# Optimization experiments

Measured on AMD Instinct MI355X. Metric: run time of the kernel, lower is better.

Reference implementation:

```python
import jax, jax.numpy as jnp
import numpy as np
from jax import lax

H = 1024        # lstm_hidden_size
V = 512         # action_vocab_size
WV = 300        # word_vec_size
S = 64          # step_num
N = 512         # entity_num


def setup_inputs() -> dict:
    key = jax.random.key(0)
    ks = jax.random.split(key, 16)
    s = 0.02
    return {
        "video_vectors": jax.random.normal(ks[0], (1, S, H), jnp.float32),
        "entity_vectors": jax.random.normal(ks[1], (N, H), jnp.float32),
        # action_selector: Linear(H,H) -> ReLU -> Dropout(eval: identity) -> Linear(H,V) -> Sigmoid
        "A1w": jax.random.normal(ks[2], (H, H), jnp.float32) * s,
        "A1b": jnp.zeros((H,), jnp.float32),
        "A2w": jax.random.normal(ks[3], (V, H), jnp.float32) * s,
        "A2b": jnp.zeros((V,), jnp.float32),
        "action_emb": jax.random.normal(ks[4], (V, WV), jnp.float32) * s,
        "W1w": jax.random.normal(ks[5], (H, H), jnp.float32) * s,
        "W1b": jnp.zeros((H,), jnp.float32),
        "W2w": jax.random.normal(ks[6], (H, H + V), jnp.float32) * s,
        "W2b": jnp.zeros((H,), jnp.float32),
        "W3w": jax.random.normal(ks[7], (3, H), jnp.float32) * s,
        "W3b": jnp.zeros((3,), jnp.float32),
        "W4w": jax.random.normal(ks[8], (1, WV), jnp.float32) * s,
        "W4b": jnp.zeros((1,), jnp.float32),
    }


def _forward(video_vectors, entity_vectors, A1w, A1b, A2w, A2b, action_emb,
             W1w, W1b, W2w, W2b, W3w, W3b, W4w, W4b):
    vv = video_vectors[0]                       # [S, H]
    n = entity_vectors.shape[0]

    def step(carry, v_ac):
        ev, prev_ent_attn = carry               # ev: [N, H], prev: [N]
        # action selector (dropout is identity in eval)
        h = jax.nn.relu(v_ac @ A1w.T + A1b)
        ac_prob = jax.nn.sigmoid(h @ A2w.T + A2b)        # [V]
        bar_ft = (ac_prob / ac_prob.sum()) @ action_emb  # [WV]
        hat_ht = jax.nn.relu(v_ac @ W1w.T + W1b)         # [H]
        w2v = jnp.concatenate([hat_ht, ac_prob]) @ W2w.T + W2b  # [H]
        ent_prob = jax.nn.sigmoid(ev @ w2v)              # [N]
        choice = jax.nn.softmax(hat_ht @ W3w.T + W3b)    # [3]
        attn = choice[0] * ent_prob + choice[1] * prev_ent_attn  # (choice[2]*0)
        bar_et = (attn / attn.sum()) @ ev                # [H]
        scal = bar_ft @ W4w[0] + W4b[0]                  # scalar (W4(bar_ft))
        kt = jax.nn.relu(scal * bar_et)                  # [H]
        ev_new = attn[:, None] * kt[None, :] + (1.0 - attn)[:, None] * ev  # [N, H]
        return (ev_new, ent_prob), (ent_prob, ac_prob, bar_et, ev_new, bar_ft)

    init = (entity_vectors, jnp.zeros((n,), entity_vectors.dtype))
    _, (ent_probs, ac_probs, step_ent, step_all, step_act) = lax.scan(step, init, vv)
    return ent_probs, ac_probs, step_ent, step_all, step_act


def reference(video_vectors, entity_vectors, A1w, A1b, A2w, A2b, action_emb,
              W1w, W1b, W2w, W2b, W3w, W3b, W4w, W4b):
    return _forward(video_vectors, entity_vectors, A1w, A1b, A2w, A2b, action_emb,
                    W1w, W1b, W2w, W2b, W3w, W3b, W4w, W4b)
```

## Files before the change

### kernel.cpp

```cpp
#include <hip/hip_runtime.h>

#define H  1024
#define V  512
#define WV 300
#define S  64
#define N  512

#define WS_HALL   0
#define WS_HAT    (S*H)
#define WS_W2V    (2*S*H)
#define WS_CHOICE (3*S*H)
#define WS_SCAL   (3*S*H + 2*S)
#define WS_ACSUM  (3*S*H + 3*S)
#define WS_ACCUM  (3*S*H + 4*S)
#define WS_ASUM   (WS_ACCUM + 3*H)
#define WS_CTR    (WS_ASUM + 4)
#define WS_FLOATS (WS_CTR + 1)

#define OUT_EP   0
#define OUT_AC   (S*N)
#define OUT_SE   (S*N + S*V)
#define OUT_ALL  (OUT_SE + S*H)
#define OUT_ACT  (OUT_ALL + (size_t)S*N*H)

__device__ __forceinline__ float wave_reduce(float v) {
#pragma unroll
  for (int m = 32; m > 0; m >>= 1) v += __shfl_xor(v, m, 64);
  return v;
}
__device__ __forceinline__ float dot4(float4 a, float4 b) {
  return a.x*b.x + a.y*b.y + a.z*b.z + a.w*b.w;
}

__global__ void k_vvmats(const float* __restrict__ vv,
                         const float* __restrict__ A1w, const float* __restrict__ A1b,
                         const float* __restrict__ W1w, const float* __restrict__ W1b,
                         float* __restrict__ ws) {
  int wid  = (blockIdx.x * blockDim.x + threadIdx.x) >> 6;
  int lane = threadIdx.x & 63;
  if (wid >= 2 * S * H) return;
  int mat = wid / (S * H);
  int rem = wid - mat * S * H;
  int t = rem >> 10, j = rem & (H - 1);
  const float* w = (mat ? W1w : A1w) + (size_t)j * H;
  const float* x = vv + (size_t)t * H;
  float sum = 0.f;
#pragma unroll
  for (int c = 0; c < 4; ++c) {
    float4 a = *(const float4*)(w + c*256 + lane*4);
    float4 b = *(const float4*)(x + c*256 + lane*4);
    sum += dot4(a, b);
  }
  sum = wave_reduce(sum);
  if (lane == 0) {
    float bias = (mat ? W1b : A1b)[j];
    ws[(mat ? WS_HAT : WS_HALL) + rem] = fmaxf(sum + bias, 0.f);
  }
}

__global__ void k_ac(const float* __restrict__ ws, const float* __restrict__ A2w,
                     const float* __restrict__ A2b, float* __restrict__ out_ac) {
  int wid  = (blockIdx.x * blockDim.x + threadIdx.x) >> 6;
  int lane = threadIdx.x & 63;
  if (wid >= S * V) return;
  int t = wid >> 9, v = wid & (V - 1);
  const float* h = ws + WS_HALL + (size_t)t * H;
  const float* w = A2w + (size_t)v * H;
  float sum = 0.f;
#pragma unroll
  for (int c = 0; c < 4; ++c) {
    float4 a = *(const float4*)(w + c*256 + lane*4);
    float4 b = *(const float4*)(h + c*256 + lane*4);
    sum += dot4(a, b);
  }
  sum = wave_reduce(sum);
  if (lane == 0) out_ac[wid] = 1.f / (1.f + __expf(-(sum + A2b[v])));
}

__global__ void k_choice(const float* __restrict__ ws_ro, const float* __restrict__ out_ac,
                         const float* __restrict__ W3w, const float* __restrict__ W3b,
                         float* __restrict__ ws) {
  int t = blockIdx.x, tid = threadIdx.x;
  const float* hat = ws_ro + WS_HAT + (size_t)t * H;
  float4 h4 = *(const float4*)(hat + tid * 4);
  float p[4];
#pragma unroll
  for (int r = 0; r < 3; ++r) {
    float4 w4 = *(const float4*)(W3w + (size_t)r * H + tid * 4);
    p[r] = dot4(h4, w4);
  }
  const float* ac = out_ac + (size_t)t * V;
  p[3] = ac[tid * 2] + ac[tid * 2 + 1];
  __shared__ float red[4][256];
#pragma unroll
  for (int q = 0; q < 4; ++q) red[q][tid] = p[q];
  __syncthreads();
  for (int sft = 128; sft > 0; sft >>= 1) {
    if (tid < sft) {
#pragma unroll
      for (int q = 0; q < 4; ++q) red[q][tid] += red[q][tid + sft];
    }
    __syncthreads();
  }
  if (tid == 0) {
    float l0 = red[0][0] + W3b[0], l1 = red[1][0] + W3b[1], l2 = red[2][0] + W3b[2];
    float m  = fmaxf(l0, fmaxf(l1, l2));
    float e0 = __expf(l0 - m), e1 = __expf(l1 - m), e2 = __expf(l2 - m);
    float inv = 1.f / (e0 + e1 + e2);
    ws[WS_CHOICE + t * 2]     = e0 * inv;
    ws[WS_CHOICE + t * 2 + 1] = e1 * inv;
    ws[WS_ACSUM + t]          = red[3][0];
  }
}

__global__ void k_w2v(const float* __restrict__ ws_ro, const float* __restrict__ out_ac,
                      const float* __restrict__ W2w, const float* __restrict__ W2b,
                      float* __restrict__ ws) {
  int wid  = (blockIdx.x * blockDim.x + threadIdx.x) >> 6;
  int lane = threadIdx.x & 63;
  if (wid >= S * H) return;
  int t = wid >> 10, j = wid & (H - 1);
  const float* w   = W2w + (size_t)j * (H + V);
  const float* hat = ws_ro + WS_HAT + (size_t)t * H;
  const float* ac  = out_ac + (size_t)t * V;
  float sum = 0.f;
#pragma unroll
  for (int c = 0; c < 4; ++c) {
    float4 a = *(const float4*)(w + c*256 + lane*4);
    float4 b = *(const float4*)(hat + c*256 + lane*4);
    sum += dot4(a, b);
  }
#pragma unroll
  for (int c = 0; c < 2; ++c) {
    float4 a = *(const float4*)(w + H + c*256 + lane*4);
    float4 b = *(const float4*)(ac + c*256 + lane*4);
    sum += dot4(a, b);
  }
  sum = wave_reduce(sum);
  if (lane == 0) ws[WS_W2V + wid] = sum + W2b[j];
}

__global__ void k_barft(const float* __restrict__ out_ac, const float* __restrict__ emb,
                        const float* __restrict__ ws_ro, float* __restrict__ out_act) {
  int wid  = (blockIdx.x * blockDim.x + threadIdx.x) >> 6;
  int lane = threadIdx.x & 63;
  if (wid >= S * WV) return;
  int t = wid / WV, w = wid - t * WV;
  const float* ac = out_ac + (size_t)t * V;
  float sum = 0.f;
  for (int v = lane; v < V; v += 64) sum += ac[v] * emb[(size_t)v * WV + w];
  sum = wave_reduce(sum);
  if (lane == 0) out_act[wid] = sum / ws_ro[WS_ACSUM + t];
}

__global__ void k_scal(const float* __restrict__ out_act, const float* __restrict__ W4w,
                       const float* __restrict__ W4b, float* __restrict__ ws) {
  int wid  = (blockIdx.x * blockDim.x + threadIdx.x) >> 6;
  int lane = threadIdx.x & 63;
  if (wid >= S) return;
  const float* bf = out_act + (size_t)wid * WV;
  float sum = 0.f;
  for (int w = lane; w < WV; w += 64) sum += bf[w] * W4w[w];
  sum = wave_reduce(sum);
  if (lane == 0) ws[WS_SCAL + wid] = sum + W4b[0];
}

__global__ __launch_bounds__(256) void k_seq(
    const float* __restrict__ ev0, const float* __restrict__ ws,
    float* __restrict__ accum, float* __restrict__ asum, unsigned* __restrict__ ctr,
    float* __restrict__ out_ep, float* __restrict__ out_se, float* __restrict__ out_all) {
  const int g = blockIdx.x, tid = threadIdx.x;
  const int lane = tid & 63, wv = tid >> 6;
  const int col = tid * 4;
  __shared__ float attnS[8], prevS[8], red[8][4];
  if (tid < 8) prevS[tid] = 0.f;
  float4 ev[8];
#pragma unroll
  for (int r = 0; r < 8; ++r)
    ev[r] = *(const float4*)(ev0 + (size_t)(g * 8 + r) * H + col);
  __syncthreads();
  unsigned target = 0;
  for (int t = 0; t < S; ++t) {
    const float4 w4 = *(const float4*)(ws + WS_W2V + (size_t)t * H + col);
    float dp[8];
#pragma unroll
    for (int r = 0; r < 8; ++r) dp[r] = dot4(ev[r], w4);
#pragma unroll
    for (int r = 0; r < 8; ++r) {
#pragma unroll
      for (int m = 32; m > 0; m >>= 1) dp[r] += __shfl_xor(dp[r], m, 64);
    }
    if (lane == 0) {
#pragma unroll
      for (int r = 0; r < 8; ++r) red[r][wv] = dp[r];
    }
    __syncthreads();
    if (tid < 8) {
      float d  = red[tid][0] + red[tid][1] + red[tid][2] + red[tid][3];
      float ep = 1.f / (1.f + __expf(-d));
      out_ep[(size_t)t * N + g * 8 + tid] = ep;
      float a = ws[WS_CHOICE + 2 * t] * ep + ws[WS_CHOICE + 2 * t + 1] * prevS[tid];
      prevS[tid] = ep;
      attnS[tid] = a;
    }
    __syncthreads();
    float at[8];
#pragma unroll
    for (int r = 0; r < 8; ++r) at[r] = attnS[r];
    float4 pv = make_float4(0.f, 0.f, 0.f, 0.f);
#pragma unroll
    for (int r = 0; r < 8; ++r) {
      pv.x += at[r] * ev[r].x; pv.y += at[r] * ev[r].y;
      pv.z += at[r] * ev[r].z; pv.w += at[r] * ev[r].w;
    }
    float* acc = accum + (t % 3) * H;
    atomicAdd(acc + col + 0, pv.x);
    atomicAdd(acc + col + 1, pv.y);
    atomicAdd(acc + col + 2, pv.z);
    atomicAdd(acc + col + 3, pv.w);
    if (tid == 0) {
      float pa = 0.f;
#pragma unroll
      for (int r = 0; r < 8; ++r) pa += at[r];
      atomicAdd(asum + (t % 3), pa);
    }
    __threadfence();
    __syncthreads();
    target += (unsigned)gridDim.x;
    if (tid == 0) {
      __hip_atomic_fetch_add(ctr, 1u, __ATOMIC_RELEASE, __HIP_MEMORY_SCOPE_AGENT);
      while (__hip_atomic_load(ctr, __ATOMIC_ACQUIRE, __HIP_MEMORY_SCOPE_AGENT) < target)
        __builtin_amdgcn_s_sleep(2);
    }
    __syncthreads();
    float asv = __hip_atomic_load(asum + (t % 3), __ATOMIC_RELAXED, __HIP_MEMORY_SCOPE_AGENT);
    float4 pvs;
    pvs.x = __hip_atomic_load(acc + col + 0, __ATOMIC_RELAXED, __HIP_MEMORY_SCOPE_AGENT);
    pvs.y = __hip_atomic_load(acc + col + 1, __ATOMIC_RELAXED, __HIP_MEMORY_SCOPE_AGENT);
    pvs.z = __hip_atomic_load(acc + col + 2, __ATOMIC_RELAXED, __HIP_MEMORY_SCOPE_AGENT);
    pvs.w = __hip_atomic_load(acc + col + 3, __ATOMIC_RELAXED, __HIP_MEMORY_SCOPE_AGENT);
    float inv = 1.f / asv;
    float4 bar = make_float4(pvs.x * inv, pvs.y * inv, pvs.z * inv, pvs.w * inv);
    float sc = ws[WS_SCAL + t];
    float4 kt = make_float4(fmaxf(sc * bar.x, 0.f), fmaxf(sc * bar.y, 0.f),
                            fmaxf(sc * bar.z, 0.f), fmaxf(sc * bar.w, 0.f));
    if (g == 0) *(float4*)(out_se + (size_t)t * H + col) = bar;
    if (tid < 16)
      __hip_atomic_store(accum + ((t + 2) % 3) * H + g * 16 + tid, 0.f,
                         __ATOMIC_RELAXED, __HIP_MEMORY_SCOPE_AGENT);
    if (g == 0 && tid == 16)
      __hip_atomic_store(asum + ((t + 2) % 3), 0.f, __ATOMIC_RELAXED, __HIP_MEMORY_SCOPE_AGENT);
    float* outp = out_all + (size_t)t * N * H;
#pragma unroll
    for (int r = 0; r < 8; ++r) {
      float a = at[r];
      ev[r].x = a * kt.x + (1.f - a) * ev[r].x;
      ev[r].y = a * kt.y + (1.f - a) * ev[r].y;
      ev[r].z = a * kt.z + (1.f - a) * ev[r].z;
      ev[r].w = a * kt.w + (1.f - a) * ev[r].w;
      *(float4*)(outp + (size_t)(g * 8 + r) * H + col) = ev[r];
    }
  }
}

extern "C" void kernel_launch(void* const* d_in, const int* in_sizes, int n_in,
                              void* d_out, int out_size, void* d_ws, size_t ws_size,
                              hipStream_t stream) {
  const float* vv  = (const float*)d_in[0];
  const float* ev0 = (const float*)d_in[1];
  const float* A1w = (const float*)d_in[2];
  const float* A1b = (const float*)d_in[3];
  const float* A2w = (const float*)d_in[4];
  const float* A2b = (const float*)d_in[5];
  const float* emb = (const float*)d_in[6];
  const float* W1w = (const float*)d_in[7];
  const float* W1b = (const float*)d_in[8];
  const float* W2w = (const float*)d_in[9];
  const float* W2b = (const float*)d_in[10];
  const float* W3w = (const float*)d_in[11];
  const float* W3b = (const float*)d_in[12];
  const float* W4w = (const float*)d_in[13];
  const float* W4b = (const float*)d_in[14];

  float* ws  = (float*)d_ws;
  float* out = (float*)d_out;
  float* out_ep  = out + OUT_EP;
  float* out_ac  = out + OUT_AC;
  float* out_se  = out + OUT_SE;
  float* out_all = out + OUT_ALL;
  float* out_act = out + OUT_ACT;

  hipMemsetAsync(ws + WS_ACCUM, 0, (size_t)(3 * H + 4 + 1) * sizeof(float), stream);

  k_vvmats<<<(2 * S * H) / 4, 256, 0, stream>>>(vv, A1w, A1b, W1w, W1b, ws);
  k_ac    <<<(S * V) / 4,     256, 0, stream>>>(ws, A2w, A2b, out_ac);
  k_choice<<<S,               256, 0, stream>>>(ws, out_ac, W3w, W3b, ws);
  k_w2v   <<<(S * H) / 4,     256, 0, stream>>>(ws, out_ac, W2w, W2b, ws);
  k_barft <<<(S * WV + 3) / 4, 256, 0, stream>>>(out_ac, emb, ws, out_act);
  k_scal  <<<(S + 3) / 4,     256, 0, stream>>>(out_act, W4w, W4b, ws);
  k_seq   <<<64,              256, 0, stream>>>(ev0, ws,
                                                ws + WS_ACCUM, ws + WS_ASUM,
                                                (unsigned*)(ws + WS_CTR),
                                                out_ep, out_se, out_all);
}
```

Before: 1.177 ms.

## Tile precompute GEMMs in LDS and move ev output writes to a separate kernel

```diff
diff --git a/kernel.cpp b/kernel.cpp
--- a/kernel.cpp
+++ b/kernel.cpp
@@ -7,15 +7,16 @@
 #define N  512
 
 #define WS_HALL   0
-#define WS_HAT    (S*H)
-#define WS_W2V    (2*S*H)
-#define WS_CHOICE (3*S*H)
-#define WS_SCAL   (3*S*H + 2*S)
-#define WS_ACSUM  (3*S*H + 3*S)
-#define WS_ACCUM  (3*S*H + 4*S)
+#define WS_CAT    (S*H)
+#define WS_W2V    (WS_CAT + S*1536)
+#define WS_CHOICE (WS_W2V + S*H)
+#define WS_SCAL   (WS_CHOICE + 2*S)
+#define WS_ACSUM  (WS_SCAL + S)
+#define WS_KT     (WS_ACSUM + S)
+#define WS_ATT    (WS_KT + S*H)
+#define WS_ACCUM  (WS_ATT + S*N)
 #define WS_ASUM   (WS_ACCUM + 3*H)
 #define WS_CTR    (WS_ASUM + 4)
-#define WS_FLOATS (WS_CTR + 1)
 
 #define OUT_EP   0
 #define OUT_AC   (S*N)
@@ -32,56 +33,72 @@
   return a.x*b.x + a.y*b.y + a.z*b.z + a.w*b.w;
 }
 
-__global__ void k_vvmats(const float* __restrict__ vv,
-                         const float* __restrict__ A1w, const float* __restrict__ A1b,
-                         const float* __restrict__ W1w, const float* __restrict__ W1b,
-                         float* __restrict__ ws) {
-  int wid  = (blockIdx.x * blockDim.x + threadIdx.x) >> 6;
-  int lane = threadIdx.x & 63;
-  if (wid >= 2 * S * H) return;
-  int mat = wid / (S * H);
-  int rem = wid - mat * S * H;
-  int t = rem >> 10, j = rem & (H - 1);
-  const float* w = (mat ? W1w : A1w) + (size_t)j * H;
-  const float* x = vv + (size_t)t * H;
-  float sum = 0.f;
-#pragma unroll
-  for (int c = 0; c < 4; ++c) {
-    float4 a = *(const float4*)(w + c*256 + lane*4);
-    float4 b = *(const float4*)(x + c*256 + lane*4);
-    sum += dot4(a, b);
-  }
-  sum = wave_reduce(sum);
-  if (lane == 0) {
-    float bias = (mat ? W1b : A1b)[j];
-    ws[(mat ? WS_HAT : WS_HALL) + rem] = fmaxf(sum + bias, 0.f);
-  }
-}
-
-__global__ void k_ac(const float* __restrict__ ws, const float* __restrict__ A2w,
-                     const float* __restrict__ A2b, float* __restrict__ out_ac) {
-  int wid  = (blockIdx.x * blockDim.x + threadIdx.x) >> 6;
-  int lane = threadIdx.x & 63;
-  if (wid >= S * V) return;
-  int t = wid >> 9, v = wid & (V - 1);
-  const float* h = ws + WS_HALL + (size_t)t * H;
-  const float* w = A2w + (size_t)v * H;
-  float sum = 0.f;
-#pragma unroll
-  for (int c = 0; c < 4; ++c) {
-    float4 a = *(const float4*)(w + c*256 + lane*4);
-    float4 b = *(const float4*)(h + c*256 + lane*4);
-    sum += dot4(a, b);
-  }
-  sum = wave_reduce(sum);
-  if (lane == 0) out_ac[wid] = 1.f / (1.f + __expf(-(sum + A2b[v])));
-}
-
-__global__ void k_choice(const float* __restrict__ ws_ro, const float* __restrict__ out_ac,
+#define KC 64
+__global__ __launch_bounds__(256) void gemmNT(
+    const float* __restrict__ X, int ldx,
+    const float* __restrict__ W, const float* __restrict__ bias,
+    int K, int act,
+    float* __restrict__ out1, int ld1,
+    float* __restrict__ out2, int ld2) {
+  __shared__ float Xs[64][KC + 4];
+  __shared__ float Ws[64][KC + 4];
+  const int tid = threadIdx.x;
+  const int tm = tid >> 5, tn = tid & 31;
+  const int jbase = blockIdx.x * 64;
+  float acc[8][2];
+#pragma unroll
+  for (int i = 0; i < 8; ++i) acc[i][0] = acc[i][1] = 0.f;
+  const int lr = tid >> 2;
+  const int lc = (tid & 3) * 16;
+  for (int k0 = 0; k0 < K; k0 += KC) {
+    const float4* xp = (const float4*)(X + (size_t)lr * ldx + k0 + lc);
+    const float4* wp = (const float4*)(W + (size_t)(jbase + lr) * K + k0 + lc);
+    float4 xv0 = xp[0], xv1 = xp[1], xv2 = xp[2], xv3 = xp[3];
+    float4 wv0 = wp[0], wv1 = wp[1], wv2 = wp[2], wv3 = wp[3];
+    __syncthreads();
+    *(float4*)&Xs[lr][lc +  0] = xv0; *(float4*)&Xs[lr][lc +  4] = xv1;
+    *(float4*)&Xs[lr][lc +  8] = xv2; *(float4*)&Xs[lr][lc + 12] = xv3;
+    *(float4*)&Ws[lr][lc +  0] = wv0; *(float4*)&Ws[lr][lc +  4] = wv1;
+    *(float4*)&Ws[lr][lc +  8] = wv2; *(float4*)&Ws[lr][lc + 12] = wv3;
+    __syncthreads();
+#pragma unroll
+    for (int kk = 0; kk < KC; kk += 4) {
+      float4 w0 = *(const float4*)&Ws[tn][kk];
+      float4 w1 = *(const float4*)&Ws[tn + 32][kk];
+#pragma unroll
+      for (int i = 0; i < 8; ++i) {
+        float4 x = *(const float4*)&Xs[tm * 8 + i][kk];
+        acc[i][0] += dot4(x, w0);
+        acc[i][1] += dot4(x, w1);
+      }
+    }
+  }
+  const int j0 = jbase + tn, j1 = jbase + tn + 32;
+  const float b0 = bias[j0], b1 = bias[j1];
+#pragma unroll
+  for (int i = 0; i < 8; ++i) {
+    const int r = tm * 8 + i;
+    float v0 = acc[i][0] + b0;
+    float v1 = acc[i][1] + b1;
+    if (act == 1) { v0 = fmaxf(v0, 0.f); v1 = fmaxf(v1, 0.f); }
+    else if (act == 2) {
+      v0 = 1.f / (1.f + __expf(-v0));
+      v1 = 1.f / (1.f + __expf(-v1));
+    }
+    out1[(size_t)r * ld1 + j0] = v0;
+    out1[(size_t)r * ld1 + j1] = v1;
+    if (out2) {
+      out2[(size_t)r * ld2 + j0] = v0;
+      out2[(size_t)r * ld2 + j1] = v1;
+    }
+  }
+}
+
+__global__ void k_choice(const float* __restrict__ cat, const float* __restrict__ out_ac,
                          const float* __restrict__ W3w, const float* __restrict__ W3b,
                          float* __restrict__ ws) {
   int t = blockIdx.x, tid = threadIdx.x;
-  const float* hat = ws_ro + WS_HAT + (size_t)t * H;
+  const float* hat = cat + (size_t)t * 1536;
   float4 h4 = *(const float4*)(hat + tid * 4);
   float p[4];
 #pragma unroll
@@ -113,62 +130,45 @@
   }
 }
 
-__global__ void k_w2v(const float* __restrict__ ws_ro, const float* __restrict__ out_ac,
-                      const float* __restrict__ W2w, const float* __restrict__ W2b,
-                      float* __restrict__ ws) {
-  int wid  = (blockIdx.x * blockDim.x + threadIdx.x) >> 6;
-  int lane = threadIdx.x & 63;
-  if (wid >= S * H) return;
-  int t = wid >> 10, j = wid & (H - 1);
-  const float* w   = W2w + (size_t)j * (H + V);
-  const float* hat = ws_ro + WS_HAT + (size_t)t * H;
-  const float* ac  = out_ac + (size_t)t * V;
-  float sum = 0.f;
-#pragma unroll
-  for (int c = 0; c < 4; ++c) {
-    float4 a = *(const float4*)(w + c*256 + lane*4);
-    float4 b = *(const float4*)(hat + c*256 + lane*4);
-    sum += dot4(a, b);
-  }
-#pragma unroll
-  for (int c = 0; c < 2; ++c) {
-    float4 a = *(const float4*)(w + H + c*256 + lane*4);
-    float4 b = *(const float4*)(ac + c*256 + lane*4);
-    sum += dot4(a, b);
-  }
-  sum = wave_reduce(sum);
-  if (lane == 0) ws[WS_W2V + wid] = sum + W2b[j];
-}
-
-__global__ void k_barft(const float* __restrict__ out_ac, const float* __restrict__ emb,
-                        const float* __restrict__ ws_ro, float* __restrict__ out_act) {
-  int wid  = (blockIdx.x * blockDim.x + threadIdx.x) >> 6;
-  int lane = threadIdx.x & 63;
-  if (wid >= S * WV) return;
-  int t = wid / WV, w = wid - t * WV;
+__global__ __launch_bounds__(256) void k_barft(
+    const float* __restrict__ out_ac, const float* __restrict__ emb,
+    const float* __restrict__ ws_ro, const float* __restrict__ W4w,
+    const float* __restrict__ W4b, float* __restrict__ out_act,
+    float* __restrict__ ws) {
+  int t = blockIdx.x, tid = threadIdx.x;
+  __shared__ float acS[V];
   const float* ac = out_ac + (size_t)t * V;
-  float sum = 0.f;
-  for (int v = lane; v < V; v += 64) sum += ac[v] * emb[(size_t)v * WV + w];
-  sum = wave_reduce(sum);
-  if (lane == 0) out_act[wid] = sum / ws_ro[WS_ACSUM + t];
-}
-
-__global__ void k_scal(const float* __restrict__ out_act, const float* __restrict__ W4w,
-                       const float* __restrict__ W4b, float* __restrict__ ws) {
-  int wid  = (blockIdx.x * blockDim.x + threadIdx.x) >> 6;
-  int lane = threadIdx.x & 63;
-  if (wid >= S) return;
-  const float* bf = out_act + (size_t)wid * WV;
-  float sum = 0.f;
-  for (int w = lane; w < WV; w += 64) sum += bf[w] * W4w[w];
-  sum = wave_reduce(sum);
-  if (lane == 0) ws[WS_SCAL + wid] = sum + W4b[0];
+  acS[tid] = ac[tid];
+  acS[tid + 256] = ac[tid + 256];
+  __syncthreads();
+  float s0 = 0.f, s1 = 0.f;
+  const int w0 = tid, w1 = 256 + tid;
+  for (int v = 0; v < V; ++v) {
+    float a = acS[v];
+    const float* er = emb + (size_t)v * WV;
+    s0 += a * er[w0];
+    if (tid < WV - 256) s1 += a * er[w1];
+  }
+  float inv = 1.f / ws_ro[WS_ACSUM + t];
+  s0 *= inv; s1 *= inv;
+  out_act[(size_t)t * WV + w0] = s0;
+  if (tid < WV - 256) out_act[(size_t)t * WV + w1] = s1;
+  float p = s0 * W4w[w0] + (tid < WV - 256 ? s1 * W4w[w1] : 0.f);
+  __shared__ float red[256];
+  red[tid] = p;
+  __syncthreads();
+  for (int s = 128; s > 0; s >>= 1) {
+    if (tid < s) red[tid] += red[tid + s];
+    __syncthreads();
+  }
+  if (tid == 0) ws[WS_SCAL + t] = red[0] + W4b[0];
 }
 
 __global__ __launch_bounds__(256) void k_seq(
     const float* __restrict__ ev0, const float* __restrict__ ws,
     float* __restrict__ accum, float* __restrict__ asum, unsigned* __restrict__ ctr,
-    float* __restrict__ out_ep, float* __restrict__ out_se, float* __restrict__ out_all) {
+    float* __restrict__ att, float* __restrict__ ktb,
+    float* __restrict__ out_ep, float* __restrict__ out_se) {
   const int g = blockIdx.x, tid = threadIdx.x;
   const int lane = tid & 63, wv = tid >> 6;
   const int col = tid * 4;
@@ -202,6 +202,7 @@
       float a = ws[WS_CHOICE + 2 * t] * ep + ws[WS_CHOICE + 2 * t + 1] * prevS[tid];
       prevS[tid] = ep;
       attnS[tid] = a;
+      att[(size_t)t * N + g * 8 + tid] = a;
     }
     __syncthreads();
     float at[8];
@@ -224,7 +225,6 @@
       for (int r = 0; r < 8; ++r) pa += at[r];
       atomicAdd(asum + (t % 3), pa);
     }
-    __threadfence();
     __syncthreads();
     target += (unsigned)gridDim.x;
     if (tid == 0) {
@@ -244,13 +244,15 @@
     float sc = ws[WS_SCAL + t];
     float4 kt = make_float4(fmaxf(sc * bar.x, 0.f), fmaxf(sc * bar.y, 0.f),
                             fmaxf(sc * bar.z, 0.f), fmaxf(sc * bar.w, 0.f));
-    if (g == 0) *(float4*)(out_se + (size_t)t * H + col) = bar;
+    if (g == 0) {
+      *(float4*)(out_se + (size_t)t * H + col) = bar;
+      *(float4*)(ktb + (size_t)t * H + col) = kt;
+    }
     if (tid < 16)
       __hip_atomic_store(accum + ((t + 2) % 3) * H + g * 16 + tid, 0.f,
                          __ATOMIC_RELAXED, __HIP_MEMORY_SCOPE_AGENT);
     if (g == 0 && tid == 16)
       __hip_atomic_store(asum + ((t + 2) % 3), 0.f, __ATOMIC_RELAXED, __HIP_MEMORY_SCOPE_AGENT);
-    float* outp = out_all + (size_t)t * N * H;
 #pragma unroll
     for (int r = 0; r < 8; ++r) {
       float a = at[r];
@@ -258,8 +260,27 @@
       ev[r].y = a * kt.y + (1.f - a) * ev[r].y;
       ev[r].z = a * kt.z + (1.f - a) * ev[r].z;
       ev[r].w = a * kt.w + (1.f - a) * ev[r].w;
-      *(float4*)(outp + (size_t)(g * 8 + r) * H + col) = ev[r];
-    }
+    }
+  }
+}
+
+__global__ __launch_bounds__(256) void k_recon(
+    const float* __restrict__ ev0, const float* __restrict__ att,
+    const float* __restrict__ ktb, float* __restrict__ out_all) {
+  const int n = blockIdx.x, tid = threadIdx.x;
+  const int col = tid * 4;
+  __shared__ float aS[S];
+  if (tid < S) aS[tid] = att[(size_t)tid * N + n];
+  float4 v = *(const float4*)(ev0 + (size_t)n * H + col);
+  __syncthreads();
+  for (int t = 0; t < S; ++t) {
+    float a = aS[t];
+    float4 k4 = *(const float4*)(ktb + (size_t)t * H + col);
+    v.x = a * k4.x + (1.f - a) * v.x;
+    v.y = a * k4.y + (1.f - a) * v.y;
+    v.z = a * k4.z + (1.f - a) * v.z;
+    v.w = a * k4.w + (1.f - a) * v.w;
+    *(float4*)(out_all + ((size_t)t * N + n) * H + col) = v;
   }
 }
 
@@ -289,17 +310,18 @@
   float* out_se  = out + OUT_SE;
   float* out_all = out + OUT_ALL;
   float* out_act = out + OUT_ACT;
-
-  hipMemsetAsync(ws + WS_ACCUM, 0, (size_t)(3 * H + 4 + 1) * sizeof(float), stream);
-
-  k_vvmats<<<(2 * S * H) / 4, 256, 0, stream>>>(vv, A1w, A1b, W1w, W1b, ws);
-  k_ac    <<<(S * V) / 4,     256, 0, stream>>>(ws, A2w, A2b, out_ac);
-  k_choice<<<S,               256, 0, stream>>>(ws, out_ac, W3w, W3b, ws);
-  k_w2v   <<<(S * H) / 4,     256, 0, stream>>>(ws, out_ac, W2w, W2b, ws);
-  k_barft <<<(S * WV + 3) / 4, 256, 0, stream>>>(out_ac, emb, ws, out_act);
-  k_scal  <<<(S + 3) / 4,     256, 0, stream>>>(out_act, W4w, W4b, ws);
-  k_seq   <<<64,              256, 0, stream>>>(ev0, ws,
-                                                ws + WS_ACCUM, ws + WS_ASUM,
-                                                (unsigned*)(ws + WS_CTR),
-                                                out_ep, out_se, out_all);
-}
+  float* cat = ws + WS_CAT;
+
+  hipMemsetAsync(ws + WS_ACCUM, 0, (size_t)(3 * H + 5) * sizeof(float), stream);
+
+  gemmNT<<<16, 256, 0, stream>>>(vv, H, A1w, A1b, H, 1, ws + WS_HALL, H, (float*)nullptr, 0);
+  gemmNT<<<16, 256, 0, stream>>>(vv, H, W1w, W1b, H, 1, cat, 1536, (float*)nullptr, 0);
+  gemmNT<<<8, 256, 0, stream>>>(ws + WS_HALL, H, A2w, A2b, H, 2, out_ac, V, cat + H, 1536);
+  k_choice<<<S, 256, 0, stream>>>(cat, out_ac, W3w, W3b, ws);
+  gemmNT<<<16, 256, 0, stream>>>(cat, 1536, W2w, W2b, 1536, 0, ws + WS_W2V, H, (float*)nullptr, 0);
+  k_barft<<<S, 256, 0, stream>>>(out_ac, emb, ws, W4w, W4b, out_act, ws);
+  k_seq<<<64, 256, 0, stream>>>(ev0, ws, ws + WS_ACCUM, ws + WS_ASUM,
+                                (unsigned*)(ws + WS_CTR),
+                                ws + WS_ATT, ws + WS_KT, out_ep, out_se);
+  k_recon<<<N, 256, 0, stream>>>(ev0, ws + WS_ATT, ws + WS_KT, out_all);
+}
```

After: 1.380 ms. 17.2% more time.
